# Optimization experiments

Hardware: AMD Instinct MI355X
Metric: run time of the kernel (lower is better)

## Reference

```python
import jax, jax.numpy as jnp
import numpy as np


def setup_inputs() -> dict:
    key = jax.random.key(0)
    ks = jax.random.split(key, 3)
    B, d_in, d_latent = 8192, 768, 12288
    x = jax.random.normal(ks[0], (B, d_in), dtype=jnp.float32)
    # kaiming_normal fan_in relu: std = sqrt(2/d_in)
    W_enc = jax.random.normal(ks[1], (d_latent, d_in), dtype=jnp.float32) * np.sqrt(2.0 / d_in)
    b_enc = jnp.zeros((d_latent,), dtype=jnp.float32)
    # xavier_normal: std = sqrt(2/(d_in+d_latent))
    W_dec = jax.random.normal(ks[2], (d_in, d_latent), dtype=jnp.float32) * np.sqrt(2.0 / (d_in + d_latent))
    b_dec = jnp.zeros((d_in,), dtype=jnp.float32)
    b_pre = jnp.zeros((d_in,), dtype=jnp.float32)
    return {"x": x, "b_pre": b_pre, "W_enc": W_enc, "b_enc": b_enc,
            "W_dec": W_dec, "b_dec": b_dec, "k": 64}


def reference(x, b_pre, W_enc, b_enc, W_dec, b_dec, k):
    # encode: a = (x - b_pre) @ W_enc.T + b_enc   -> (B, d_latent)
    x0 = x - b_pre
    a = jnp.einsum('bi,li->bl', x0, W_enc) + b_enc
    # topk activation (mode='value', nonneg=True): relu then keep k largest
    a_relu = jax.nn.relu(a)
    topk_val, topk_idx = jax.lax.top_k(a_relu, k)  # (B, k)
    B = a.shape[0]
    rows = jnp.arange(B)[:, None]
    z = jnp.zeros_like(a).at[rows, topk_idx].set(topk_val)
    # decode: x_hat = z @ W_dec.T + b_dec
    x_hat = jnp.einsum('bl,il->bi', z, W_dec) + b_dec
    return (x_hat, z, a)
```

## Files before the change

kernel.cpp:

```cpp
#include <hip/hip_runtime.h>

#define DIN 768
#define DL  12288
#define CAP 320
#define CAP2 512
#define BCAP 2048
#define TCAND 2.9f
#define MARGIN 0.03f
#define UB 0.015f
#define UMAX 64
#define KMAX 128

typedef __attribute__((ext_vector_type(8))) _Float16 half8;
typedef __attribute__((ext_vector_type(4))) _Float16 half4v;
typedef __attribute__((ext_vector_type(4))) float f32x4;

__device__ __forceinline__ void gl_lds16(const void* g, void* s) {
  __builtin_amdgcn_global_load_lds(
      (const __attribute__((address_space(1))) unsigned int*)g,
      (__attribute__((address_space(3))) unsigned int*)s, 16, 0, 0);
}
__device__ __forceinline__ void wait_lgkm0_fence() {
  asm volatile("s_waitcnt lgkmcnt(0)" ::: "memory");
  __builtin_amdgcn_sched_barrier(0);
}
__device__ __forceinline__ void wait_vm0() {
  asm volatile("s_waitcnt vmcnt(0)" ::: "memory");
}

#define NBX (8192 * DIN / 1024)
#define NBW (DL * DIN / 1024)
#define NBT ((DL / 32) * (DIN / 32))

template <int ZMETA>
__global__ __launch_bounds__(256) void k_prep(
    const float* __restrict__ x, const float* __restrict__ b_pre,
    const float* __restrict__ W_enc, const float* __restrict__ W_dec,
    _Float16* __restrict__ Ah, _Float16* __restrict__ Bh, _Float16* __restrict__ WT,
    int* __restrict__ meta)
{
  const int b = blockIdx.x, tid = threadIdx.x;
  if (b < NBX) {
    const int i4 = b * 256 + tid;
    const int col4 = (i4 % (DIN / 4)) * 4;
    const float4 xv = *(const float4*)&x[(size_t)i4 * 4];
    const float4 bp = *(const float4*)&b_pre[col4];
    half4v o;
    o.x = (_Float16)(xv.x - bp.x);
    o.y = (_Float16)(xv.y - bp.y);
    o.z = (_Float16)(xv.z - bp.z);
    o.w = (_Float16)(xv.w - bp.w);
    *(half4v*)&Ah[(size_t)i4 * 4] = o;
  } else if (b < NBX + NBW) {
    const int i4 = (b - NBX) * 256 + tid;
    const float4 wv = *(const float4*)&W_enc[(size_t)i4 * 4];
    half4v o;
    o.x = (_Float16)wv.x; o.y = (_Float16)wv.y;
    o.z = (_Float16)wv.z; o.w = (_Float16)wv.w;
    *(half4v*)&Bh[(size_t)i4 * 4] = o;
  } else if (b < NBX + NBW + NBT) {
    const int idx = b - NBX - NBW;
    const int c0 = (idx % (DL / 32)) * 32;
    const int r0 = (idx / (DL / 32)) * 32;
    const int xx = tid & 31, yy = tid >> 5;
    __shared__ float t[32][33];
#pragma unroll
    for (int dy = 0; dy < 32; dy += 8)
      t[yy + dy][xx] = W_dec[(size_t)(r0 + yy + dy) * DL + c0 + xx];
    __syncthreads();
#pragma unroll
    for (int dy = 0; dy < 32; dy += 8)
      WT[(size_t)(c0 + yy + dy) * DIN + r0 + xx] = (_Float16)t[xx][yy + dy];
  } else if (ZMETA) {
    const int4 z4 = {0, 0, 0, 0};
#pragma unroll
    for (int s = 0; s < 16; ++s) ((int4*)meta)[tid * 16 + s] = z4;
  }
}

#define BM 256
#define BN 256
#define BKE 64
#define NKT (DIN / BKE)

template <int EMIT>
__global__ __launch_bounds__(512) void k_encode_f16(
    const _Float16* __restrict__ Ah, const _Float16* __restrict__ Bh,
    const float* __restrict__ b_enc, float* __restrict__ aout,
    int* __restrict__ cnt, int2* __restrict__ cand, float* __restrict__ zout)
{
  __shared__ _Float16 sA[2][BM][BKE];
  __shared__ _Float16 sB[2][BN][BKE];
  __shared__ int s_bcnt;
  const int tid = threadIdx.x, wave = tid >> 6, lane = tid & 63;
  const int wm = wave >> 2, wn = wave & 3;
  const int fr = lane & 15, fc = lane >> 4;

  const int q = ((8192 / BM) * (DL / BN)) >> 3;
  const int wg = (blockIdx.x & 7) * q + (blockIdx.x >> 3);
  const int bm = (wg / (DL / BN)) * BM;
  const int bn = (wg % (DL / BN)) * BN;

  const int lrow = lane >> 3;
  const int lcol = ((lane & 7) ^ lrow) << 3;
  const _Float16* gA = Ah + (size_t)(bm + lrow) * DIN + lcol;
  const _Float16* gB = Bh + (size_t)(bn + lrow) * DIN + lcol;

  f32x4 acc[8][4];
#pragma unroll
  for (int i = 0; i < 8; ++i)
#pragma unroll
    for (int j = 0; j < 4; ++j) acc[i][j] = f32x4{0.f, 0.f, 0.f, 0.f};

#define STAGE_TILE(buf, tt)                                                      \
  {                                                                              \
    _Pragma("unroll")                                                            \
    for (int s4 = 0; s4 < 4; ++s4) {                                             \
      const int s8 = (wave + s4 * 8) * 8;                                        \
      gl_lds16(gA + (size_t)s8 * DIN + (tt) * BKE, &sA[buf][s8][0]);             \
      gl_lds16(gB + (size_t)s8 * DIN + (tt) * BKE, &sB[buf][s8][0]);             \
    }                                                                            \
  }

#define LOADQ(p, mh, nh)                                                         \
  {                                                                              \
    const char* bA = (const char*)&sA[p][0][0];                                  \
    const char* bB = (const char*)&sB[p][0][0];                                  \
    _Pragma("unroll")                                                            \
    for (int i = 0; i < 4; ++i)                                                  \
      _Pragma("unroll")                                                          \
      for (int ks = 0; ks < 2; ++ks) {                                           \
        const int row = wm * 128 + ((mh) * 4 + i) * 16 + fr;                     \
        const int ph = (ks * 4 + fc) ^ (fr & 7);                                 \
        af[i][ks] = *(const half8*)(bA + row * (BKE * 2) + ph * 16);             \
      }                                                                          \
    _Pragma("unroll")                                                            \
    for (int j = 0; j < 2; ++j)                                                  \
      _Pragma("unroll")                                                          \
      for (int ks = 0; ks < 2; ++ks) {                                           \
        const int row = wn * 64 + ((nh) * 2 + j) * 16 + fr;                      \
        const int ph = (ks * 4 + fc) ^ (fr & 7);                                 \
        bf[j][ks] = *(const half8*)(bB + row * (BKE * 2) + ph * 16);             \
      }                                                                          \
  }

#define MFMAQ(mh, nh)                                                            \
  __builtin_amdgcn_s_setprio(1);                                                 \
  _Pragma("unroll")                                                              \
  for (int i = 0; i < 4; ++i)                                                    \
    _Pragma("unroll")                                                            \
    for (int j = 0; j < 2; ++j)                                                  \
      _Pragma("unroll")                                                          \
      for (int ks = 0; ks < 2; ++ks)                                             \
        acc[(mh) * 4 + i][(nh) * 2 + j] = __builtin_amdgcn_mfma_f32_16x16x32_f16( \
            af[i][ks], bf[j][ks], acc[(mh) * 4 + i][(nh) * 2 + j], 0, 0, 0);     \
  __builtin_amdgcn_s_setprio(0);

  half8 af[4][2], bf[2][2];

  STAGE_TILE(0, 0)
  if (EMIT) {
    const float4 zz4 = {0.f, 0.f, 0.f, 0.f};
#pragma unroll
    for (int s = 0; s < 32; ++s)
      *(float4*)&zout[(size_t)(bm + s * 8 + wave) * DL + bn + lane * 4] = zz4;
    asm volatile("s_waitcnt vmcnt(32)" ::: "memory");
  } else {
    wait_vm0();
  }
  __builtin_amdgcn_s_barrier();

#pragma unroll 1
  for (int t = 0; t < NKT; ++t) {
    const int p = t & 1;
    LOADQ(p, 0, 0)
    if (t + 1 < NKT) STAGE_TILE(p ^ 1, t + 1)
    __builtin_amdgcn_s_barrier();
    wait_lgkm0_fence();
    MFMAQ(0, 0)
    __builtin_amdgcn_s_barrier();
    LOADQ(p, 0, 1)
    __builtin_amdgcn_s_barrier();
    wait_lgkm0_fence();
    MFMAQ(0, 1)
    __builtin_amdgcn_s_barrier();
    LOADQ(p, 1, 0)
    __builtin_amdgcn_s_barrier();
    wait_lgkm0_fence();
    MFMAQ(1, 0)
    __builtin_amdgcn_s_barrier();
    LOADQ(p, 1, 1)
    wait_vm0();
    __builtin_amdgcn_s_barrier();
    wait_lgkm0_fence();
    MFMAQ(1, 1)
    __builtin_amdgcn_s_barrier();
  }

  unsigned* pk   = (unsigned*)&sA[0][0][0];
  float*    pv   = (float*)&sA[1][0][0];
  int*      lcnt = (int*)&sB[0][0][0];
  if (EMIT) {
    if (tid == 0) s_bcnt = 0;
    if (tid < 256) lcnt[tid] = 0;
    __syncthreads();
  }

#pragma unroll
  for (int j = 0; j < 4; ++j) {
    const int col = bn + wn * 64 + j * 16 + fr;
    const float be = b_enc[col];
#pragma unroll
    for (int i = 0; i < 8; ++i) {
      const int row0 = bm + wm * 128 + i * 16 + fc * 4;
#pragma unroll
      for (int r = 0; r < 4; ++r) {
        const float v = acc[i][j][r] + be;
        aout[(size_t)(row0 + r) * DL + col] = v;
        if (EMIT && v > TCAND) {
          const int lr = wm * 128 + i * 16 + fc * 4 + r;
          const int lc = wn * 64 + j * 16 + fr;
          const int p2 = atomicAdd(&s_bcnt, 1);
          if (p2 < BCAP) {
            pk[p2] = ((unsigned)lr << 8) | (unsigned)lc;
            pv[p2] = v;
          }
          atomicAdd(&lcnt[lr], 1);
        }
      }
    }
  }

  if (EMIT) {
    __syncthreads();
    const int total = s_bcnt;
    if (total > BCAP) {
      if (tid < 256) atomicAdd(&cnt[bm + tid], CAP2);
    } else {
      if (tid < 256) {
        const int c = lcnt[tid];
        lcnt[tid] = c ? atomicAdd(&cnt[bm + tid], c) : 0;
      }
      __syncthreads();
      for (int e = tid; e < total; e += 512) {
        const unsigned pkv = pk[e];
        const int lr = pkv >> 8, lc = pkv & 255u;
        const int p2 = atomicAdd(&lcnt[lr], 1);
        if (p2 < CAP2) {
          int2 o; o.x = __float_as_int(pv[e]); o.y = bn + lc;
          cand[(size_t)(bm + lr) * CAP2 + p2] = o;
        }
      }
    }
  }
#undef STAGE_TILE
#undef LOADQ
#undef MFMAQ
}

__global__ __launch_bounds__(512) void k_fast(
    const int* __restrict__ cnt, const int2* __restrict__ cand,
    const float* __restrict__ x, const float* __restrict__ b_pre,
    const float* __restrict__ W, const float* __restrict__ b_enc,
    const int* __restrict__ kp, const _Float16* __restrict__ WT,
    const float* __restrict__ b_dec, float* __restrict__ z,
    float* __restrict__ xhat, int* __restrict__ flag)
{
  const int row = blockIdx.x, tid = threadIdx.x;
  const int wave = tid >> 6, lane = tid & 63;
  const int kk = min(max(kp[0], 1), KMAX);
  float* zr = z + (size_t)row * DL;

  __shared__ float cv[CAP2];
  __shared__ int ci[CAP2];
  __shared__ double x0[DIN];
  __shared__ float s_ak;
  __shared__ int s_nw, s_ucnt;
  __shared__ int uidx[UMAX];
  __shared__ double uex[UMAX];
  __shared__ int widx[KMAX];
  __shared__ float wval[KMAX];

  const int Craw = cnt[row];
  const int C = min(Craw, CAP2);
  for (int i = tid; i < C; i += 512) {
    const int2 p = cand[(size_t)row * CAP2 + i];
    cv[i] = __int_as_float(p.x);
    ci[i] = p.y;
  }
  for (int i = tid; i < DIN; i += 512)
    x0[i] = (double)x[(size_t)row * DIN + i] - (double)b_pre[i];
  if (tid == 0) { s_ak = -1e30f; s_nw = 0; s_ucnt = 0; }
  __syncthreads();

  bool defic = (Craw >= CAP2) || (C < kk);
  if (!defic) {
    if (tid < C) {
      const float mv = cv[tid];
      const int mi = ci[tid];
      int r = 0;
      for (int j = 0; j < C; ++j) {
        const float fj = cv[j];
        if (fj > mv || (fj == mv && ci[j] < mi)) ++r;
      }
      if (r == kk - 1) s_ak = mv;
    }
    __syncthreads();
    if (s_ak - UB <= TCAND) defic = true;
  } else {
    __syncthreads();
  }
  if (defic) {
    if (tid == 0) flag[row] = 1;
    return;
  }
  const float ak = s_ak;

  if (tid < C) {
    const float mv = cv[tid];
    if (mv > ak + UB) {
      const int p = atomicAdd(&s_nw, 1);
      widx[p] = ci[tid]; wval[p] = mv;
    } else if (mv >= ak - UB) {
      const int p = atomicAdd(&s_ucnt, 1);
      if (p < UMAX) uidx[p] = ci[tid];
    }
  }
  __syncthreads();
  const int nci = s_nw;
  const int ucnt = min(s_ucnt, UMAX);

  for (int c = wave; c < ucnt; c += 8) {
    const int idx = uidx[c];
    const float* wrow = W + (size_t)idx * DIN;
    double s = 0.0;
#pragma unroll
    for (int it = 0; it < DIN / 64; ++it)
      s = fma(x0[lane + it * 64], (double)wrow[lane + it * 64], s);
#pragma unroll
    for (int mm = 32; mm; mm >>= 1) s += __shfl_xor(s, mm);
    if (lane == 0) {
      const double e = s + (double)b_enc[idx];
      uex[c] = e > 0.0 ? e : 0.0;
    }
  }
  __syncthreads();

  const int utake = min(kk - nci, ucnt);
  if (tid < ucnt) {
    const double mv = uex[tid];
    const int mi = uidx[tid];
    int r = 0;
    for (int j = 0; j < ucnt; ++j) {
      const double fj = uex[j];
      if (fj > mv || (fj == mv && uidx[j] < mi)) ++r;
    }
    if (r < utake) {
      const int p = atomicAdd(&s_nw, 1);
      widx[p] = mi; wval[p] = (float)mv;
    }
  }
  __syncthreads();
  const int nW = s_nw;

  if (tid < nW) zr[widx[tid]] = wval[tid];

  if (tid < 192) {
    float4 acc = ((const float4*)b_dec)[tid];
    for (int j = 0; j < nW; ++j) {
      const float vv = wval[j];
      const half4v w4 = *(const half4v*)(WT + (size_t)widx[j] * DIN + tid * 4);
      acc.x = fmaf(vv, (float)w4.x, acc.x);
      acc.y = fmaf(vv, (float)w4.y, acc.y);
      acc.z = fmaf(vv, (float)w4.z, acc.z);
      acc.w = fmaf(vv, (float)w4.w, acc.w);
    }
    ((float4*)(xhat + (size_t)row * DIN))[tid] = acc;
  }
}

template <int FORCE_ALL, int ZERO_Z>
__global__ __launch_bounds__(512) void k_full(
    const float* __restrict__ a, const float* __restrict__ x,
    const float* __restrict__ b_pre, const float* __restrict__ W,
    const float* __restrict__ b_enc, const int* __restrict__ kp,
    const _Float16* __restrict__ WT, const float* __restrict__ b_dec,
    float* __restrict__ z, float* __restrict__ xhat, const int* __restrict__ flag)
{
  const int row = blockIdx.x, tid = threadIdx.x;
  if (!FORCE_ALL && flag[row] == 0) return;
  const int wave = tid >> 6, lane = tid & 63;
  const int kk = min(max(kp[0], 1), KMAX);
  const float* ar = a + (size_t)row * DL;
  float* zr = z + (size_t)row * DL;

  __shared__ unsigned hist[4][512];
  __shared__ float s_wmax[8];
  __shared__ unsigned s_wsuf[8];
  __shared__ float s_Tm;
  __shared__ int s_cnt;
  __shared__ int cidx[CAP];
  __shared__ float caf[CAP];
  __shared__ double x0[DIN];
  __shared__ float s_ak;
  __shared__ int s_ucnt, s_nw;
  __shared__ int uidx[UMAX];
  __shared__ double uex[UMAX];
  __shared__ int widx[KMAX];
  __shared__ float wval[KMAX];

  float4 v[6];
#pragma unroll
  for (int j = 0; j < 6; ++j) {
    float4 t4 = ((const float4*)ar)[tid + 512 * j];
    t4.x = fmaxf(t4.x, 0.f); t4.y = fmaxf(t4.y, 0.f);
    t4.z = fmaxf(t4.z, 0.f); t4.w = fmaxf(t4.w, 0.f);
    v[j] = t4;
    if (ZERO_Z) {
      const float4 zz = {0.f, 0.f, 0.f, 0.f};
      ((float4*)zr)[tid + 512 * j] = zz;
    }
  }
  for (int i = tid; i < DIN; i += 512)
    x0[i] = (double)x[(size_t)row * DIN + i] - (double)b_pre[i];
  float m = 0.f;
#pragma unroll
  for (int j = 0; j < 6; ++j)
    m = fmaxf(m, fmaxf(fmaxf(v[j].x, v[j].y), fmaxf(v[j].z, v[j].w)));
#pragma unroll
  for (int off = 32; off; off >>= 1) m = fmaxf(m, __shfl_xor(m, off));
  if (lane == 0) s_wmax[wave] = m;
  if (tid == 0) { s_cnt = 0; s_Tm = -1.f; s_ak = -1e30f; s_ucnt = 0; s_nw = 0; }
  __syncthreads();
  float rmax = s_wmax[0];
#pragma unroll
  for (int w2 = 1; w2 < 8; ++w2) rmax = fmaxf(rmax, s_wmax[w2]);

  float Tm;
  if (rmax <= 0.f) {
    Tm = 1e30f;
  } else {
    const float scale = 512.f / rmax;
    unsigned need = (unsigned)kk;
    bool found = false;
    for (int phase = 0; phase < 2 && !found; ++phase) {
      for (int i = tid; i < 4 * 512; i += 512) (&hist[0][0])[i] = 0u;
      __syncthreads();
      unsigned* h = hist[wave & 3];
      const float sc = (phase == 0) ? scale : scale * 8.f;
#pragma unroll
      for (int j = 0; j < 6; ++j) {
        const float vv[4] = {v[j].x, v[j].y, v[j].z, v[j].w};
#pragma unroll
        for (int e = 0; e < 4; ++e) {
          const float val = vv[e];
          if (val > 0.f) {
            const float fb = val * scale;
            if (phase == 0) {
              if (fb >= 64.f) atomicAdd(&h[min(511, (int)fb)], 1u);
            } else {
              if (fb < 64.f) atomicAdd(&h[min(511, (int)(val * sc))], 1u);
            }
          }
        }
      }
      __syncthreads();
      const unsigned st = hist[0][tid] + hist[1][tid] + hist[2][tid] + hist[3][tid];
      unsigned s = st;
#pragma unroll
      for (int off = 1; off < 64; off <<= 1) {
        const unsigned o = __shfl_down(s, off);
        if (lane + off < 64) s += o;
      }
      if (lane == 0) s_wsuf[wave] = s;
      __syncthreads();
      unsigned above_w = 0, total = 0;
#pragma unroll
      for (int w2 = 0; w2 < 8; ++w2) {
        total += s_wsuf[w2];
        if (w2 > wave) above_w += s_wsuf[w2];
      }
      const unsigned inc = s + above_w;
      const unsigned excl = inc - st;
      if (total >= need) {
        if (inc >= need && excl < need)
          s_Tm = (float)tid / sc - MARGIN;
        found = true;
      } else {
        need -= total;
      }
      __syncthreads();
    }
    Tm = s_Tm;
  }

#pragma unroll
  for (int j = 0; j < 6; ++j) {
    const float vv[4] = {v[j].x, v[j].y, v[j].z, v[j].w};
#pragma unroll
    for (int e = 0; e < 4; ++e) {
      if (vv[e] > 0.f && vv[e] >= Tm) {
        const int p = atomicAdd(&s_cnt, 1);
        if (p < CAP) { cidx[p] = (tid + 512 * j) * 4 + e; caf[p] = vv[e]; }
      }
    }
  }
  __syncthreads();
  const int C = min(s_cnt, CAP);

  if (C > kk) {
    if (tid < C) {
      const float mv = caf[tid];
      const int mi = cidx[tid];
      int r = 0;
      for (int j = 0; j < C; ++j) {
        const float fj = caf[j];
        if (fj > mv || (fj == mv && cidx[j] < mi)) ++r;
      }
      if (r == kk - 1) s_ak = mv;
    }
    __syncthreads();
  }
  const float ak = s_ak;

  if (tid < C) {
    const float mv = caf[tid];
    if (C <= kk || mv > ak + UB) {
      const int p = atomicAdd(&s_nw, 1);
      widx[p] = cidx[tid]; wval[p] = mv;
    } else if (mv >= ak - UB) {
      const int p = atomicAdd(&s_ucnt, 1);
      if (p < UMAX) uidx[p] = cidx[tid];
    }
  }
  __syncthreads();
  const int nci = s_nw;
  const int ucnt = min(s_ucnt, UMAX);

  for (int c = wave; c < ucnt; c += 8) {
    const int idx = uidx[c];
    const float* wrow = W + (size_t)idx * DIN;
    double s = 0.0;
#pragma unroll
    for (int it = 0; it < DIN / 64; ++it)
      s = fma(x0[lane + it * 64], (double)wrow[lane + it * 64], s);
#pragma unroll
    for (int mm = 32; mm; mm >>= 1) s += __shfl_xor(s, mm);
    if (lane == 0) {
      const double e = s + (double)b_enc[idx];
      uex[c] = e > 0.0 ? e : 0.0;
    }
  }
  __syncthreads();

  const int utake = min(kk - nci, ucnt);
  if (tid < ucnt) {
    const double mv = uex[tid];
    const int mi = uidx[tid];
    int r = 0;
    for (int j = 0; j < ucnt; ++j) {
      const double fj = uex[j];
      if (fj > mv || (fj == mv && uidx[j] < mi)) ++r;
    }
    if (r < utake) {
      const int p = atomicAdd(&s_nw, 1);
      widx[p] = mi; wval[p] = (float)mv;
    }
  }
  __syncthreads();
  const int nW = s_nw;

  if (tid < nW) zr[widx[tid]] = wval[tid];

  if (tid < 192) {
    float4 acc = ((const float4*)b_dec)[tid];
    for (int j = 0; j < nW; ++j) {
      const float vv = wval[j];
      const half4v w4 = *(const half4v*)(WT + (size_t)widx[j] * DIN + tid * 4);
      acc.x = fmaf(vv, (float)w4.x, acc.x);
      acc.y = fmaf(vv, (float)w4.y, acc.y);
      acc.z = fmaf(vv, (float)w4.z, acc.z);
      acc.w = fmaf(vv, (float)w4.w, acc.w);
    }
    ((float4*)(xhat + (size_t)row * DIN))[tid] = acc;
  }
}

extern "C" void kernel_launch(void* const* d_in, const int* in_sizes, int n_in,
                              void* d_out, int out_size, void* d_ws, size_t ws_size,
                              hipStream_t stream)
{
  const float* x     = (const float*)d_in[0];
  const float* b_pre = (const float*)d_in[1];
  const float* W_enc = (const float*)d_in[2];
  const float* b_enc = (const float*)d_in[3];
  const float* W_dec = (const float*)d_in[4];
  const float* b_dec = (const float*)d_in[5];
  const int*   kp    = (const int*)d_in[6];
  const int M = in_sizes[0] / DIN;

  float* xhat = (float*)d_out;
  float* z    = xhat + (size_t)M * DIN;
  float* a    = z + (size_t)M * DL;

  const bool bigws = ws_size >= ((size_t)192 << 20);

  if (bigws) {
    int*      cnt  = (int*)d_ws;
    int*      flag = (int*)d_ws + M;
    int2*     cand = (int2*)((char*)d_ws + ((size_t)1 << 20));
    _Float16* WT16 = (_Float16*)((char*)d_ws + ((size_t)40 << 20));
    _Float16* Ah   = (_Float16*)((char*)d_ws + ((size_t)64 << 20));
    _Float16* Bh   = (_Float16*)((char*)d_ws + ((size_t)96 << 20));

    k_prep<1><<<NBX + NBW + NBT + 1, 256, 0, stream>>>(x, b_pre, W_enc, W_dec,
                                                       Ah, Bh, WT16, cnt);
    k_encode_f16<1><<<(M / BM) * (DL / BN), 512, 0, stream>>>(Ah, Bh, b_enc, a,
                                                              cnt, cand, z);
    k_fast<<<M, 512, 0, stream>>>(cnt, cand, x, b_pre, W_enc, b_enc, kp, WT16, b_dec,
                                  z, xhat, flag);
    k_full<0, 0><<<M, 512, 0, stream>>>(a, x, b_pre, W_enc, b_enc, kp, WT16, b_dec,
                                        z, xhat, flag);
  } else {
    _Float16* WT16 = (_Float16*)z;
    _Float16* Ah   = (_Float16*)(z + (size_t)12 * 1024 * 1024);
    _Float16* Bh   = (_Float16*)(z + (size_t)20 * 1024 * 1024);

    k_prep<0><<<NBX + NBW + NBT, 256, 0, stream>>>(x, b_pre, W_enc, W_dec,
                                                   Ah, Bh, WT16, nullptr);
    k_encode_f16<0><<<(M / BM) * (DL / BN), 512, 0, stream>>>(Ah, Bh, b_enc, a,
                                                              nullptr, nullptr, nullptr);
    k_full<1, 1><<<M, 512, 0, stream>>>(a, x, b_pre, W_enc, b_enc, kp, WT16, b_dec,
                                        z, xhat, nullptr);
  }
}
```

Before: 700.6 us.

## Move z zeroing to k_fast, reorder MFMA quadrants, per-wave candidate buffers

Zeroing of the z output moves out of the encode GEMM prologue and into the per-row k_fast kernel, so the GEMM no longer issues that store traffic. The inner loop now keeps both B-fragment halves in registers and reuses the second A half for two MFMA quadrants, cutting one LDS load phase and one barrier pair per k-tile at the cost of extra VGPRs. Candidate collection uses per-wave counters and buffers instead of one block-wide shared atomic, which reduces LDS atomic contention. This risks overflowing more often when a single wave exceeds its 256-entry cap.

```diff
diff --git a/kernel.cpp b/kernel.cpp
--- a/kernel.cpp
+++ b/kernel.cpp
@@ -4,7 +4,7 @@
 #define DL  12288
 #define CAP 320
 #define CAP2 512
-#define BCAP 2048
+#define WCAP 256
 #define TCAND 2.9f
 #define MARGIN 0.03f
 #define UB 0.015f
@@ -87,11 +87,12 @@
 __global__ __launch_bounds__(512) void k_encode_f16(
     const _Float16* __restrict__ Ah, const _Float16* __restrict__ Bh,
     const float* __restrict__ b_enc, float* __restrict__ aout,
-    int* __restrict__ cnt, int2* __restrict__ cand, float* __restrict__ zout)
+    int* __restrict__ cnt, int2* __restrict__ cand)
 {
   __shared__ _Float16 sA[2][BM][BKE];
   __shared__ _Float16 sB[2][BN][BKE];
-  __shared__ int s_bcnt;
+  __shared__ int s_bcnt8[8];
+  __shared__ int s_ovf;
   const int tid = threadIdx.x, wave = tid >> 6, lane = tid & 63;
   const int wm = wave >> 2, wn = wave & 3;
   const int fr = lane & 15, fc = lane >> 4;
@@ -122,10 +123,9 @@
     }                                                                            \
   }
 
-#define LOADQ(p, mh, nh)                                                         \
+#define LOAD_AF(p, mh)                                                           \
   {                                                                              \
     const char* bA = (const char*)&sA[p][0][0];                                  \
-    const char* bB = (const char*)&sB[p][0][0];                                  \
     _Pragma("unroll")                                                            \
     for (int i = 0; i < 4; ++i)                                                  \
       _Pragma("unroll")                                                          \
@@ -134,13 +134,17 @@
         const int ph = (ks * 4 + fc) ^ (fr & 7);                                 \
         af[i][ks] = *(const half8*)(bA + row * (BKE * 2) + ph * 16);             \
       }                                                                          \
+  }
+#define LOAD_BF(p, nh)                                                           \
+  {                                                                              \
+    const char* bB = (const char*)&sB[p][0][0];                                  \
     _Pragma("unroll")                                                            \
     for (int j = 0; j < 2; ++j)                                                  \
       _Pragma("unroll")                                                          \
       for (int ks = 0; ks < 2; ++ks) {                                           \
         const int row = wn * 64 + ((nh) * 2 + j) * 16 + fr;                      \
         const int ph = (ks * 4 + fc) ^ (fr & 7);                                 \
-        bf[j][ks] = *(const half8*)(bB + row * (BKE * 2) + ph * 16);             \
+        bf[nh][j][ks] = *(const half8*)(bB + row * (BKE * 2) + ph * 16);         \
       }                                                                          \
   }
 
@@ -153,47 +157,36 @@
       _Pragma("unroll")                                                          \
       for (int ks = 0; ks < 2; ++ks)                                             \
         acc[(mh) * 4 + i][(nh) * 2 + j] = __builtin_amdgcn_mfma_f32_16x16x32_f16( \
-            af[i][ks], bf[j][ks], acc[(mh) * 4 + i][(nh) * 2 + j], 0, 0, 0);     \
+            af[i][ks], bf[nh][j][ks], acc[(mh) * 4 + i][(nh) * 2 + j], 0, 0, 0); \
   __builtin_amdgcn_s_setprio(0);
 
-  half8 af[4][2], bf[2][2];
+  half8 af[4][2], bf[2][2][2];
 
   STAGE_TILE(0, 0)
-  if (EMIT) {
-    const float4 zz4 = {0.f, 0.f, 0.f, 0.f};
-#pragma unroll
-    for (int s = 0; s < 32; ++s)
-      *(float4*)&zout[(size_t)(bm + s * 8 + wave) * DL + bn + lane * 4] = zz4;
-    asm volatile("s_waitcnt vmcnt(32)" ::: "memory");
-  } else {
-    wait_vm0();
-  }
+  wait_vm0();
   __builtin_amdgcn_s_barrier();
 
 #pragma unroll 1
   for (int t = 0; t < NKT; ++t) {
     const int p = t & 1;
-    LOADQ(p, 0, 0)
+    LOAD_AF(p, 0)
+    LOAD_BF(p, 0)
     if (t + 1 < NKT) STAGE_TILE(p ^ 1, t + 1)
     __builtin_amdgcn_s_barrier();
     wait_lgkm0_fence();
     MFMAQ(0, 0)
     __builtin_amdgcn_s_barrier();
-    LOADQ(p, 0, 1)
+    LOAD_BF(p, 1)
     __builtin_amdgcn_s_barrier();
     wait_lgkm0_fence();
     MFMAQ(0, 1)
     __builtin_amdgcn_s_barrier();
-    LOADQ(p, 1, 0)
-    __builtin_amdgcn_s_barrier();
-    wait_lgkm0_fence();
-    MFMAQ(1, 0)
-    __builtin_amdgcn_s_barrier();
-    LOADQ(p, 1, 1)
+    LOAD_AF(p, 1)
     wait_vm0();
     __builtin_amdgcn_s_barrier();
     wait_lgkm0_fence();
     MFMAQ(1, 1)
+    MFMAQ(1, 0)
     __builtin_amdgcn_s_barrier();
   }
 
@@ -201,7 +194,8 @@
   float*    pv   = (float*)&sA[1][0][0];
   int*      lcnt = (int*)&sB[0][0][0];
   if (EMIT) {
-    if (tid == 0) s_bcnt = 0;
+    if (tid < 8) s_bcnt8[tid] = 0;
+    if (tid == 0) s_ovf = 0;
     if (tid < 256) lcnt[tid] = 0;
     __syncthreads();
   }
@@ -220,10 +214,10 @@
         if (EMIT && v > TCAND) {
           const int lr = wm * 128 + i * 16 + fc * 4 + r;
           const int lc = wn * 64 + j * 16 + fr;
-          const int p2 = atomicAdd(&s_bcnt, 1);
-          if (p2 < BCAP) {
-            pk[p2] = ((unsigned)lr << 8) | (unsigned)lc;
-            pv[p2] = v;
+          const int p2 = atomicAdd(&s_bcnt8[wave], 1);
+          if (p2 < WCAP) {
+            pk[wave * WCAP + p2] = ((unsigned)lr << 8) | (unsigned)lc;
+            pv[wave * WCAP + p2] = v;
           }
           atomicAdd(&lcnt[lr], 1);
         }
@@ -233,8 +227,9 @@
 
   if (EMIT) {
     __syncthreads();
-    const int total = s_bcnt;
-    if (total > BCAP) {
+    if (tid < 8 && s_bcnt8[tid] > WCAP) s_ovf = 1;
+    __syncthreads();
+    if (s_ovf) {
       if (tid < 256) atomicAdd(&cnt[bm + tid], CAP2);
     } else {
       if (tid < 256) {
@@ -242,19 +237,24 @@
         lcnt[tid] = c ? atomicAdd(&cnt[bm + tid], c) : 0;
       }
       __syncthreads();
-      for (int e = tid; e < total; e += 512) {
-        const unsigned pkv = pk[e];
-        const int lr = pkv >> 8, lc = pkv & 255u;
-        const int p2 = atomicAdd(&lcnt[lr], 1);
-        if (p2 < CAP2) {
-          int2 o; o.x = __float_as_int(pv[e]); o.y = bn + lc;
-          cand[(size_t)(bm + lr) * CAP2 + p2] = o;
+#pragma unroll 1
+      for (int w = 0; w < 8; ++w) {
+        const int tw = s_bcnt8[w];
+        for (int e = tid; e < tw; e += 512) {
+          const unsigned pkv = pk[w * WCAP + e];
+          const int lr = pkv >> 8, lc = pkv & 255u;
+          const int p2 = atomicAdd(&lcnt[lr], 1);
+          if (p2 < CAP2) {
+            int2 o; o.x = __float_as_int(pv[w * WCAP + e]); o.y = bn + lc;
+            cand[(size_t)(bm + lr) * CAP2 + p2] = o;
+          }
         }
       }
     }
   }
 #undef STAGE_TILE
-#undef LOADQ
+#undef LOAD_AF
+#undef LOAD_BF
 #undef MFMAQ
 }
 
@@ -280,6 +280,10 @@
   __shared__ double uex[UMAX];
   __shared__ int widx[KMAX];
   __shared__ float wval[KMAX];
+
+  const float4 zz = {0.f, 0.f, 0.f, 0.f};
+#pragma unroll
+  for (int j = 0; j < 6; ++j) ((float4*)zr)[tid + 512 * j] = zz;
 
   const int Craw = cnt[row];
   const int C = min(Craw, CAP2);
@@ -616,7 +620,7 @@
     k_prep<1><<<NBX + NBW + NBT + 1, 256, 0, stream>>>(x, b_pre, W_enc, W_dec,
                                                        Ah, Bh, WT16, cnt);
     k_encode_f16<1><<<(M / BM) * (DL / BN), 512, 0, stream>>>(Ah, Bh, b_enc, a,
-                                                              cnt, cand, z);
+                                                              cnt, cand);
     k_fast<<<M, 512, 0, stream>>>(cnt, cand, x, b_pre, W_enc, b_enc, kp, WT16, b_dec,
                                   z, xhat, flag);
     k_full<0, 0><<<M, 512, 0, stream>>>(a, x, b_pre, W_enc, b_enc, kp, WT16, b_dec,
@@ -629,7 +633,7 @@
     k_prep<0><<<NBX + NBW + NBT, 256, 0, stream>>>(x, b_pre, W_enc, W_dec,
                                                    Ah, Bh, WT16, nullptr);
     k_encode_f16<0><<<(M / BM) * (DL / BN), 512, 0, stream>>>(Ah, Bh, b_enc, a,
-                                                              nullptr, nullptr, nullptr);
+                                                              nullptr, nullptr);
     k_full<1, 1><<<M, 512, 0, stream>>>(a, x, b_pre, W_enc, b_enc, kp, WT16, b_dec,
                                         z, xhat, nullptr);
   }
```

Measured after the change: 630.7 us (median of 2 runs). 1.11x faster.
